# Kernel optimization log

Hardware: AMD Instinct MI355X
Metric: run time of the kernel (lower is better)

The kernel has to match this reference:

```python
import jax, jax.numpy as jnp
import numpy as np

N_NODES = 50000
N_EDGES = 500000
F_IN = 128
F_OUT = 128
N_REL = 8


def setup_inputs() -> dict:
    key = jax.random.key(0)
    ks = jax.random.split(key, 10)
    x = jax.random.normal(ks[0], (N_NODES, F_IN), dtype=jnp.float32)
    edge_index = jax.random.randint(ks[1], (2, N_EDGES), 0, N_NODES, dtype=jnp.int64)
    edge_types = jax.random.randint(ks[2], (N_EDGES,), 0, N_REL, dtype=jnp.int64)
    s = 1.0 / np.sqrt(F_IN)
    Wr = jax.random.uniform(ks[3], (N_REL, F_OUT, F_IN), jnp.float32, -s, s)  # per-relation Linear weights [out,in]
    br = jax.random.uniform(ks[4], (N_REL, F_OUT), jnp.float32, -s, s)
    Ws = jax.random.uniform(ks[5], (F_OUT, F_IN), jnp.float32, -s, s)         # self Linear
    bs = jax.random.uniform(ks[6], (F_OUT,), jnp.float32, -s, s)
    sa = 1.0 / np.sqrt(2 * F_IN)
    wa = jax.random.uniform(ks[7], (2 * F_IN,), jnp.float32, -sa, sa)         # attention Linear(2*in, 1) weight
    ba = jax.random.uniform(ks[8], (1,), jnp.float32, -sa, sa)
    return {"x": x, "edge_index": edge_index, "edge_types": edge_types,
            "Wr": Wr, "br": br, "Ws": Ws, "bs": bs, "wa": wa, "ba": ba}


def reference(x, edge_index, edge_types, Wr, br, Ws, bs, wa, ba):
    N, Fin = x.shape
    R = Wr.shape[0]
    src, tgt = edge_index[0], edge_index[1]
    # self term: self_weight(x)
    out = x @ Ws.T + bs
    # attention: sigmoid(cat(x[src], x[tgt]) @ wa + ba), decomposed per node then gathered
    a_src = x @ wa[:Fin]   # [N]
    a_tgt = x @ wa[Fin:]   # [N]
    a = jax.nn.sigmoid(a_src[src] + a_tgt[tgt] + ba[0])  # [E]
    # contribution per edge: a * (x[src] @ Wr^T + br)  =>  aggregate (a * x[src]) and a per (target, relation)
    scaled = x[src] * a[:, None]                         # [E, Fin]
    seg = tgt * R + edge_types                           # combined (target, relation) segment id
    agg = jax.ops.segment_sum(scaled, seg, num_segments=N * R).reshape(N, R, Fin)
    asum = jax.ops.segment_sum(a, seg, num_segments=N * R).reshape(N, R)
    out = out + jnp.einsum('nri,roi->no', agg, Wr) + asum @ br
    return out
```

## Files before the change

kernel.cpp:

```cpp
#include <hip/hip_runtime.h>
#include <math.h>

#define NND 50000
#define NED 500000
#define FDIM 128
#define NREL 8
#define KTOT 1152
#define MPAD 50048
#define CAP 64
#define NKC  (KTOT / 64)

typedef __attribute__((ext_vector_type(8))) short short8;
typedef __attribute__((ext_vector_type(4))) float f32x4;
typedef const void __attribute__((address_space(1)))* gptr_t;
typedef void __attribute__((address_space(3)))* lptr_t;

static __device__ __forceinline__ unsigned short f2bf(float f) {
    unsigned u = __float_as_uint(f);
    u += 0x7FFFu + ((u >> 16) & 1u);
    return (unsigned short)(u >> 16);
}
static __device__ __forceinline__ float bf2f(unsigned short b) {
    return __uint_as_float((unsigned)b << 16);
}

#define NDB   12500
#define PBB   72
#define CZB   196
#define AZB   27
__global__ void node_dots_kernel(const float* __restrict__ x,
                                 const float* __restrict__ wa,
                                 float* __restrict__ a_src,
                                 float* __restrict__ a_tgt,
                                 unsigned short* __restrict__ Abig,
                                 unsigned short* __restrict__ xb,
                                 const float* __restrict__ Ws,
                                 const float* __restrict__ Wr,
                                 unsigned short* __restrict__ Bt,
                                 int* __restrict__ counts) {
    int b = blockIdx.x;
    if (b < NDB) {
        int gid  = b * 256 + threadIdx.x;
        int node = gid >> 6;
        int lane = threadIdx.x & 63;
        float2 v = *(const float2*)(x + (size_t)node * FDIM + lane * 2);
        ushort2 vb = { f2bf(v.x), f2bf(v.y) };
        *(ushort2*)(Abig + (size_t)node * KTOT + lane * 2) = vb;
        *(ushort2*)(xb   + (size_t)node * FDIM + lane * 2) = vb;
        float s1 = v.x * wa[2 * lane]        + v.y * wa[2 * lane + 1];
        float s2 = v.x * wa[FDIM + 2 * lane] + v.y * wa[FDIM + 2 * lane + 1];
#pragma unroll
        for (int off = 32; off > 0; off >>= 1) {
            s1 += __shfl_xor(s1, off);
            s2 += __shfl_xor(s2, off);
        }
        if (lane == 0) { a_src[node] = s1; a_tgt[node] = s2; }
    } else if (b < NDB + PBB) {
        int idx0 = (b - NDB) * 2048 + threadIdx.x * 8;
        int o  = idx0 / KTOT;
        int k0 = idx0 - o * KTOT;
        unsigned short tmp[8];
#pragma unroll
        for (int j = 0; j < 8; ++j) {
            int k = k0 + j;
            float v;
            if (k < FDIM) v = Ws[o * FDIM + k];
            else {
                int r = (k - FDIM) >> 7;
                int i = (k - FDIM) & 127;
                v = Wr[((size_t)r * FDIM + o) * FDIM + i];
            }
            tmp[j] = f2bf(v);
        }
        *(short8*)(Bt + idx0) = *(short8*)tmp;
    } else if (b < NDB + PBB + CZB) {
        int i = (b - NDB - PBB) * 256 + threadIdx.x;
        if (i < NND) counts[i] = 0;
    } else {
        int i = (b - NDB - PBB - CZB) * 256 + threadIdx.x;
        float4 z = make_float4(0.f, 0.f, 0.f, 0.f);
        ((float4*)(Abig + (size_t)NND * KTOT))[i] = z;
    }
}

__global__ void scatter_kernel(const int* __restrict__ ei, const int* __restrict__ et,
                               const float* __restrict__ a_src, const float* __restrict__ a_tgt,
                               const float* __restrict__ ba,
                               int* __restrict__ counts,
                               unsigned long long* __restrict__ sorted2) {
    int e = blockIdx.x * blockDim.x + threadIdx.x;
    if (e >= NED) return;
    int src = ei[e];
    int tgt = ei[NED + e];
    int rel = et[e];
    float s = a_src[src] + a_tgt[tgt] + ba[0];
    float a = 1.0f / (1.0f + __expf(-s));
    int slot = atomicAdd(&counts[tgt], 1);
    if (slot < CAP) {
        unsigned long long pk = ((unsigned long long)__float_as_uint(a) << 32)
                              | (unsigned)((rel << 16) | src);
        sorted2[(size_t)tgt * CAP + slot] = pk;
    }
}

__global__ __launch_bounds__(256) void segsum_kernel(
        const int* __restrict__ counts, const unsigned long long* __restrict__ sorted2,
        const unsigned short* __restrict__ xb,
        unsigned short* __restrict__ Abig, float* __restrict__ asum) {
    int wid  = (blockIdx.x * blockDim.x + threadIdx.x) >> 6;
    int lane = threadIdx.x & 63;
    if (wid >= NND) return;
    int tgt = wid;
    int cnt = counts[tgt];
    if (cnt > CAP) cnt = CAP;
    const unsigned long long* seg = sorted2 + (size_t)tgt * CAP;

    float2 c0 = {0,0}, c1 = {0,0}, c2 = {0,0}, c3 = {0,0};
    float2 c4 = {0,0}, c5 = {0,0}, c6 = {0,0}, c7 = {0,0};
    float s0=0,s1=0,s2=0,s3=0,s4=0,s5=0,s6=0,s7=0;

    const ushort2* xl = (const ushort2*)xb + lane;

#define ACC(PK, W) {                                                    \
        float a  = __uint_as_float((unsigned)((PK) >> 32));             \
        int  rel = (int)(((PK) >> 16) & 0xF);                           \
        float vx = bf2f((W).x), vy = bf2f((W).y);                       \
        switch (rel) {                                                  \
            case 0: c0.x += a*vx; c0.y += a*vy; s0 += a; break;         \
            case 1: c1.x += a*vx; c1.y += a*vy; s1 += a; break;         \
            case 2: c2.x += a*vx; c2.y += a*vy; s2 += a; break;         \
            case 3: c3.x += a*vx; c3.y += a*vy; s3 += a; break;         \
            case 4: c4.x += a*vx; c4.y += a*vy; s4 += a; break;         \
            case 5: c5.x += a*vx; c5.y += a*vy; s5 += a; break;         \
            case 6: c6.x += a*vx; c6.y += a*vy; s6 += a; break;         \
            default: c7.x += a*vx; c7.y += a*vy; s7 += a; break;        \
        }                                                               \
    }

    int k = 0;
    if (cnt >= 4) {
        unsigned long long pk0 = seg[0];
        unsigned long long pk1 = seg[1];
        unsigned long long pk2 = seg[2];
        unsigned long long pk3 = seg[3];
        for (; k + 8 <= cnt; k += 4) {
            ushort2 w0 = xl[(size_t)(pk0 & 0xFFFF) * 64];
            ushort2 w1 = xl[(size_t)(pk1 & 0xFFFF) * 64];
            ushort2 w2 = xl[(size_t)(pk2 & 0xFFFF) * 64];
            ushort2 w3 = xl[(size_t)(pk3 & 0xFFFF) * 64];
            unsigned long long q0 = seg[k + 4];
            unsigned long long q1 = seg[k + 5];
            unsigned long long q2 = seg[k + 6];
            unsigned long long q3 = seg[k + 7];
            ACC(pk0, w0); ACC(pk1, w1); ACC(pk2, w2); ACC(pk3, w3);
            pk0 = q0; pk1 = q1; pk2 = q2; pk3 = q3;
        }
        ushort2 w0 = xl[(size_t)(pk0 & 0xFFFF) * 64];
        ushort2 w1 = xl[(size_t)(pk1 & 0xFFFF) * 64];
        ushort2 w2 = xl[(size_t)(pk2 & 0xFFFF) * 64];
        ushort2 w3 = xl[(size_t)(pk3 & 0xFFFF) * 64];
        ACC(pk0, w0); ACC(pk1, w1); ACC(pk2, w2); ACC(pk3, w3);
        k += 4;
    }
    for (; k < cnt; ++k) {
        unsigned long long pk = seg[k];
        ushort2 w = xl[(size_t)(pk & 0xFFFF) * 64];
        ACC(pk, w);
    }
#undef ACC

    unsigned short* base = Abig + (size_t)tgt * KTOT + FDIM + lane * 2;
    ushort2 w;
    w.x = f2bf(c0.x); w.y = f2bf(c0.y); *(ushort2*)(base + 0 * FDIM) = w;
    w.x = f2bf(c1.x); w.y = f2bf(c1.y); *(ushort2*)(base + 1 * FDIM) = w;
    w.x = f2bf(c2.x); w.y = f2bf(c2.y); *(ushort2*)(base + 2 * FDIM) = w;
    w.x = f2bf(c3.x); w.y = f2bf(c3.y); *(ushort2*)(base + 3 * FDIM) = w;
    w.x = f2bf(c4.x); w.y = f2bf(c4.y); *(ushort2*)(base + 4 * FDIM) = w;
    w.x = f2bf(c5.x); w.y = f2bf(c5.y); *(ushort2*)(base + 5 * FDIM) = w;
    w.x = f2bf(c6.x); w.y = f2bf(c6.y); *(ushort2*)(base + 6 * FDIM) = w;
    w.x = f2bf(c7.x); w.y = f2bf(c7.y); *(ushort2*)(base + 7 * FDIM) = w;
    if (lane == 0) {
        float* ab = asum + (size_t)tgt * NREL;
        ab[0]=s0; ab[1]=s1; ab[2]=s2; ab[3]=s3; ab[4]=s4; ab[5]=s5; ab[6]=s6; ab[7]=s7;
    }
}

__global__ __launch_bounds__(256) void mfma_gemm_kernel(
        const unsigned short* __restrict__ Abig,
        const unsigned short* __restrict__ Bt,
        const float* __restrict__ asum,
        const float* __restrict__ br,
        const float* __restrict__ bs,
        float* __restrict__ out) {
    __shared__ __align__(16) unsigned short AsB[64 * 64];
    __shared__ __align__(16) unsigned short BsB[128 * 64];
    int tid  = threadIdx.x;
    int wave = tid >> 6;
    int lane = tid & 63;
    int l15  = lane & 15;
    int lhi  = lane >> 4;
    int brow = blockIdx.x * 64;
    int wr = wave >> 1;
    int wc = wave & 1;

    f32x4 acc[2][4];
#pragma unroll
    for (int mi = 0; mi < 2; ++mi)
#pragma unroll
        for (int ni = 0; ni < 4; ++ni) acc[mi][ni] = (f32x4){0.f, 0.f, 0.f, 0.f};

    for (int kc = 0; kc < NKC; ++kc) {
#pragma unroll
        for (int q = 0; q < 2; ++q) {
            int c    = tid + q * 256;
            int trow = c >> 3;
            int csw  = (c & 7) ^ (trow & 7);
            const unsigned short* src = Abig + (size_t)(brow + trow) * KTOT + kc * 64 + csw * 8;
            __builtin_amdgcn_global_load_lds((gptr_t)src,
                (lptr_t)&AsB[wave * 512 + q * 2048], 16, 0, 0);
        }
#pragma unroll
        for (int q = 0; q < 4; ++q) {
            int c   = tid + q * 256;
            int o   = c >> 3;
            int csw = (c & 7) ^ (o & 7);
            const unsigned short* src = Bt + (size_t)o * KTOT + kc * 64 + csw * 8;
            __builtin_amdgcn_global_load_lds((gptr_t)src,
                (lptr_t)&BsB[wave * 512 + q * 2048], 16, 0, 0);
        }
        __syncthreads();
#pragma unroll
        for (int ks = 0; ks < 2; ++ks) {
            int kslot = ks * 4 + lhi;
            short8 a[2], b[4];
#pragma unroll
            for (int mi = 0; mi < 2; ++mi) {
                int row = wr * 32 + mi * 16 + l15;
                a[mi] = *(const short8*)&AsB[row * 64 + ((kslot ^ (row & 7)) << 3)];
            }
#pragma unroll
            for (int ni = 0; ni < 4; ++ni) {
                int o = wc * 64 + ni * 16 + l15;
                b[ni] = *(const short8*)&BsB[o * 64 + ((kslot ^ (o & 7)) << 3)];
            }
#pragma unroll
            for (int mi = 0; mi < 2; ++mi)
#pragma unroll
                for (int ni = 0; ni < 4; ++ni)
                    acc[mi][ni] = __builtin_amdgcn_mfma_f32_16x16x32_bf16(
                        a[mi], b[ni], acc[mi][ni], 0, 0, 0);
        }
        __syncthreads();
    }

#pragma unroll
    for (int mi = 0; mi < 2; ++mi) {
        int rowbase = brow + wr * 32 + mi * 16 + lhi * 4;
#pragma unroll
        for (int j = 0; j < 4; ++j) {
            int row = rowbase + j;
            if (row >= NND) continue;
            const float* as = asum + (size_t)row * NREL;
            float4 sa = *(const float4*)as;
            float4 sb = *(const float4*)(as + 4);
#pragma unroll
            for (int ni = 0; ni < 4; ++ni) {
                int col = wc * 64 + ni * 16 + l15;
                float v = acc[mi][ni][j] + bs[col];
                v += sa.x * br[0 * FDIM + col] + sa.y * br[1 * FDIM + col]
                   + sa.z * br[2 * FDIM + col] + sa.w * br[3 * FDIM + col];
                v += sb.x * br[4 * FDIM + col] + sb.y * br[5 * FDIM + col]
                   + sb.z * br[6 * FDIM + col] + sb.w * br[7 * FDIM + col];
                out[(size_t)row * FDIM + col] = v;
            }
        }
    }
}

extern "C" void kernel_launch(void* const* d_in, const int* in_sizes, int n_in,
                              void* d_out, int out_size, void* d_ws, size_t ws_size,
                              hipStream_t stream) {
    const float* x  = (const float*)d_in[0];
    const int*   ei = (const int*)d_in[1];
    const int*   et = (const int*)d_in[2];
    const float* Wr = (const float*)d_in[3];
    const float* br = (const float*)d_in[4];
    const float* Ws = (const float*)d_in[5];
    const float* bs = (const float*)d_in[6];
    const float* wa = (const float*)d_in[7];
    const float* ba = (const float*)d_in[8];
    float* out = (float*)d_out;
    float* ws  = (float*)d_ws;

    const size_t abigF = ((size_t)MPAD * KTOT) / 2;
    const size_t btF   = ((size_t)FDIM * KTOT) / 2;
    const size_t xbF   = ((size_t)NND * FDIM) / 2;
    size_t o = 0;
    unsigned short* Abig = (unsigned short*)(ws + o); o += abigF;
    unsigned short* Bt   = (unsigned short*)(ws + o); o += btF;
    unsigned short* xb   = (unsigned short*)(ws + o); o += xbF;
    float* asum  = ws + o; o += (size_t)NND * NREL;
    float* a_src = ws + o; o += NND;
    float* a_tgt = ws + o; o += NND;
    int*   counts = (int*)(ws + o); o += NND;
    unsigned long long* sorted2 = (unsigned long long*)(ws + o); o += 2 * (size_t)NND * CAP;
    if (ws_size < o * sizeof(float)) return;

    dim3 blk(256);

    node_dots_kernel<<<NDB + PBB + CZB + AZB, blk, 0, stream>>>(
        x, wa, a_src, a_tgt, Abig, xb, Ws, Wr, Bt, counts);
    scatter_kernel<<<(NED + 255) / 256, blk, 0, stream>>>(
        ei, et, a_src, a_tgt, ba, counts, sorted2);
    segsum_kernel<<<(NND + 3) / 4, blk, 0, stream>>>(counts, sorted2, xb, Abig, asum);
    mfma_gemm_kernel<<<MPAD / 64, blk, 0, stream>>>(Abig, Bt, asum, br, bs, out);
}
```

Before: 119.0 us.

## Transform nodes per relation before aggregation instead of aggregating then transforming

Reorders the computation so that a GEMM first produces per-node, per-relation transformed features Z = x·Wr^T + br (plus the self term), and the edge pass then gathers and sums Z rows weighted by attention. This removes the wide 1152-column Abig buffer, the per-relation register switch in the segment sum, and the separate asum·br epilogue. The GEMM now has K=128 with nine output slices instead of K=1152. In exchange it writes a large bf16 Z buffer (N×8×128), and the gather reads from a tensor eight times larger, which lowers cache locality. Bias is also rounded to bf16 per edge.

```diff
diff --git a/kernel.cpp b/kernel.cpp
--- a/kernel.cpp
+++ b/kernel.cpp
@@ -5,10 +5,9 @@
 #define NED 500000
 #define FDIM 128
 #define NREL 8
-#define KTOT 1152
+#define NSL 9
 #define MPAD 50048
 #define CAP 64
-#define NKC  (KTOT / 64)
 
 typedef __attribute__((ext_vector_type(8))) short short8;
 typedef __attribute__((ext_vector_type(4))) float f32x4;
@@ -25,18 +24,17 @@
 }
 
 #define NDB   12500
+#define XZB   3
 #define PBB   72
 #define CZB   196
-#define AZB   27
 __global__ void node_dots_kernel(const float* __restrict__ x,
                                  const float* __restrict__ wa,
                                  float* __restrict__ a_src,
                                  float* __restrict__ a_tgt,
-                                 unsigned short* __restrict__ Abig,
                                  unsigned short* __restrict__ xb,
                                  const float* __restrict__ Ws,
                                  const float* __restrict__ Wr,
-                                 unsigned short* __restrict__ Bt,
+                                 unsigned short* __restrict__ Bt2,
                                  int* __restrict__ counts) {
     int b = blockIdx.x;
     if (b < NDB) {
@@ -45,8 +43,7 @@
         int lane = threadIdx.x & 63;
         float2 v = *(const float2*)(x + (size_t)node * FDIM + lane * 2);
         ushort2 vb = { f2bf(v.x), f2bf(v.y) };
-        *(ushort2*)(Abig + (size_t)node * KTOT + lane * 2) = vb;
-        *(ushort2*)(xb   + (size_t)node * FDIM + lane * 2) = vb;
+        *(ushort2*)(xb + (size_t)node * FDIM + lane * 2) = vb;
         float s1 = v.x * wa[2 * lane]        + v.y * wa[2 * lane + 1];
         float s2 = v.x * wa[FDIM + 2 * lane] + v.y * wa[FDIM + 2 * lane + 1];
 #pragma unroll
@@ -55,31 +52,28 @@
             s2 += __shfl_xor(s2, off);
         }
         if (lane == 0) { a_src[node] = s1; a_tgt[node] = s2; }
-    } else if (b < NDB + PBB) {
-        int idx0 = (b - NDB) * 2048 + threadIdx.x * 8;
-        int o  = idx0 / KTOT;
-        int k0 = idx0 - o * KTOT;
+    } else if (b < NDB + XZB) {
+        int i = (b - NDB) * 256 + threadIdx.x;
+        float4 z = make_float4(0.f, 0.f, 0.f, 0.f);
+        ((float4*)(xb + (size_t)NND * FDIM))[i] = z;
+    } else if (b < NDB + XZB + PBB) {
+        int idx0 = (b - NDB - XZB) * 2048 + threadIdx.x * 8;
+        int o2 = idx0 >> 7;
+        int k0 = idx0 & 127;
+        int s  = o2 >> 7;
+        int o  = o2 & 127;
         unsigned short tmp[8];
 #pragma unroll
         for (int j = 0; j < 8; ++j) {
             int k = k0 + j;
-            float v;
-            if (k < FDIM) v = Ws[o * FDIM + k];
-            else {
-                int r = (k - FDIM) >> 7;
-                int i = (k - FDIM) & 127;
-                v = Wr[((size_t)r * FDIM + o) * FDIM + i];
-            }
+            float v = (s == 0) ? Ws[o * FDIM + k]
+                               : Wr[(((size_t)(s - 1) * FDIM) + o) * FDIM + k];
             tmp[j] = f2bf(v);
         }
-        *(short8*)(Bt + idx0) = *(short8*)tmp;
-    } else if (b < NDB + PBB + CZB) {
-        int i = (b - NDB - PBB) * 256 + threadIdx.x;
+        *(short8*)(Bt2 + idx0) = *(short8*)tmp;
+    } else {
+        int i = (b - NDB - XZB - PBB) * 256 + threadIdx.x;
         if (i < NND) counts[i] = 0;
-    } else {
-        int i = (b - NDB - PBB - CZB) * 256 + threadIdx.x;
-        float4 z = make_float4(0.f, 0.f, 0.f, 0.f);
-        ((float4*)(Abig + (size_t)NND * KTOT))[i] = z;
     }
 }
 
@@ -103,94 +97,12 @@
     }
 }
 
-__global__ __launch_bounds__(256) void segsum_kernel(
-        const int* __restrict__ counts, const unsigned long long* __restrict__ sorted2,
+__global__ __launch_bounds__(256) void gemm_z_kernel(
         const unsigned short* __restrict__ xb,
-        unsigned short* __restrict__ Abig, float* __restrict__ asum) {
-    int wid  = (blockIdx.x * blockDim.x + threadIdx.x) >> 6;
-    int lane = threadIdx.x & 63;
-    if (wid >= NND) return;
-    int tgt = wid;
-    int cnt = counts[tgt];
-    if (cnt > CAP) cnt = CAP;
-    const unsigned long long* seg = sorted2 + (size_t)tgt * CAP;
-
-    float2 c0 = {0,0}, c1 = {0,0}, c2 = {0,0}, c3 = {0,0};
-    float2 c4 = {0,0}, c5 = {0,0}, c6 = {0,0}, c7 = {0,0};
-    float s0=0,s1=0,s2=0,s3=0,s4=0,s5=0,s6=0,s7=0;
-
-    const ushort2* xl = (const ushort2*)xb + lane;
-
-#define ACC(PK, W) {                                                    \
-        float a  = __uint_as_float((unsigned)((PK) >> 32));             \
-        int  rel = (int)(((PK) >> 16) & 0xF);                           \
-        float vx = bf2f((W).x), vy = bf2f((W).y);                       \
-        switch (rel) {                                                  \
-            case 0: c0.x += a*vx; c0.y += a*vy; s0 += a; break;         \
-            case 1: c1.x += a*vx; c1.y += a*vy; s1 += a; break;         \
-            case 2: c2.x += a*vx; c2.y += a*vy; s2 += a; break;         \
-            case 3: c3.x += a*vx; c3.y += a*vy; s3 += a; break;         \
-            case 4: c4.x += a*vx; c4.y += a*vy; s4 += a; break;         \
-            case 5: c5.x += a*vx; c5.y += a*vy; s5 += a; break;         \
-            case 6: c6.x += a*vx; c6.y += a*vy; s6 += a; break;         \
-            default: c7.x += a*vx; c7.y += a*vy; s7 += a; break;        \
-        }                                                               \
-    }
-
-    int k = 0;
-    if (cnt >= 4) {
-        unsigned long long pk0 = seg[0];
-        unsigned long long pk1 = seg[1];
-        unsigned long long pk2 = seg[2];
-        unsigned long long pk3 = seg[3];
-        for (; k + 8 <= cnt; k += 4) {
-            ushort2 w0 = xl[(size_t)(pk0 & 0xFFFF) * 64];
-            ushort2 w1 = xl[(size_t)(pk1 & 0xFFFF) * 64];
-            ushort2 w2 = xl[(size_t)(pk2 & 0xFFFF) * 64];
-            ushort2 w3 = xl[(size_t)(pk3 & 0xFFFF) * 64];
-            unsigned long long q0 = seg[k + 4];
-            unsigned long long q1 = seg[k + 5];
-            unsigned long long q2 = seg[k + 6];
-            unsigned long long q3 = seg[k + 7];
-            ACC(pk0, w0); ACC(pk1, w1); ACC(pk2, w2); ACC(pk3, w3);
-            pk0 = q0; pk1 = q1; pk2 = q2; pk3 = q3;
-        }
-        ushort2 w0 = xl[(size_t)(pk0 & 0xFFFF) * 64];
-        ushort2 w1 = xl[(size_t)(pk1 & 0xFFFF) * 64];
-        ushort2 w2 = xl[(size_t)(pk2 & 0xFFFF) * 64];
-        ushort2 w3 = xl[(size_t)(pk3 & 0xFFFF) * 64];
-        ACC(pk0, w0); ACC(pk1, w1); ACC(pk2, w2); ACC(pk3, w3);
-        k += 4;
-    }
-    for (; k < cnt; ++k) {
-        unsigned long long pk = seg[k];
-        ushort2 w = xl[(size_t)(pk & 0xFFFF) * 64];
-        ACC(pk, w);
-    }
-#undef ACC
-
-    unsigned short* base = Abig + (size_t)tgt * KTOT + FDIM + lane * 2;
-    ushort2 w;
-    w.x = f2bf(c0.x); w.y = f2bf(c0.y); *(ushort2*)(base + 0 * FDIM) = w;
-    w.x = f2bf(c1.x); w.y = f2bf(c1.y); *(ushort2*)(base + 1 * FDIM) = w;
-    w.x = f2bf(c2.x); w.y = f2bf(c2.y); *(ushort2*)(base + 2 * FDIM) = w;
-    w.x = f2bf(c3.x); w.y = f2bf(c3.y); *(ushort2*)(base + 3 * FDIM) = w;
-    w.x = f2bf(c4.x); w.y = f2bf(c4.y); *(ushort2*)(base + 4 * FDIM) = w;
-    w.x = f2bf(c5.x); w.y = f2bf(c5.y); *(ushort2*)(base + 5 * FDIM) = w;
-    w.x = f2bf(c6.x); w.y = f2bf(c6.y); *(ushort2*)(base + 6 * FDIM) = w;
-    w.x = f2bf(c7.x); w.y = f2bf(c7.y); *(ushort2*)(base + 7 * FDIM) = w;
-    if (lane == 0) {
-        float* ab = asum + (size_t)tgt * NREL;
-        ab[0]=s0; ab[1]=s1; ab[2]=s2; ab[3]=s3; ab[4]=s4; ab[5]=s5; ab[6]=s6; ab[7]=s7;
-    }
-}
-
-__global__ __launch_bounds__(256) void mfma_gemm_kernel(
-        const unsigned short* __restrict__ Abig,
-        const unsigned short* __restrict__ Bt,
-        const float* __restrict__ asum,
+        const unsigned short* __restrict__ Bt2,
         const float* __restrict__ br,
         const float* __restrict__ bs,
+        unsigned short* __restrict__ Z,
         float* __restrict__ out) {
     __shared__ __align__(16) unsigned short AsB[64 * 64];
     __shared__ __align__(16) unsigned short BsB[128 * 64];
@@ -199,7 +111,10 @@
     int lane = tid & 63;
     int l15  = lane & 15;
     int lhi  = lane >> 4;
-    int brow = blockIdx.x * 64;
+    int bid  = blockIdx.x;
+    int mtile = bid / NSL;
+    int slice = bid - mtile * NSL;
+    int brow = mtile * 64;
     int wr = wave >> 1;
     int wc = wave & 1;
 
@@ -209,13 +124,13 @@
 #pragma unroll
         for (int ni = 0; ni < 4; ++ni) acc[mi][ni] = (f32x4){0.f, 0.f, 0.f, 0.f};
 
-    for (int kc = 0; kc < NKC; ++kc) {
+    for (int kc = 0; kc < 2; ++kc) {
 #pragma unroll
         for (int q = 0; q < 2; ++q) {
             int c    = tid + q * 256;
             int trow = c >> 3;
             int csw  = (c & 7) ^ (trow & 7);
-            const unsigned short* src = Abig + (size_t)(brow + trow) * KTOT + kc * 64 + csw * 8;
+            const unsigned short* src = xb + (size_t)(brow + trow) * FDIM + kc * 64 + csw * 8;
             __builtin_amdgcn_global_load_lds((gptr_t)src,
                 (lptr_t)&AsB[wave * 512 + q * 2048], 16, 0, 0);
         }
@@ -224,7 +139,7 @@
             int c   = tid + q * 256;
             int o   = c >> 3;
             int csw = (c & 7) ^ (o & 7);
-            const unsigned short* src = Bt + (size_t)o * KTOT + kc * 64 + csw * 8;
+            const unsigned short* src = Bt2 + ((size_t)slice * FDIM + o) * FDIM + kc * 64 + csw * 8;
             __builtin_amdgcn_global_load_lds((gptr_t)src,
                 (lptr_t)&BsB[wave * 512 + q * 2048], 16, 0, 0);
         }
@@ -253,28 +168,100 @@
         __syncthreads();
     }
 
-#pragma unroll
-    for (int mi = 0; mi < 2; ++mi) {
-        int rowbase = brow + wr * 32 + mi * 16 + lhi * 4;
-#pragma unroll
-        for (int j = 0; j < 4; ++j) {
-            int row = rowbase + j;
-            if (row >= NND) continue;
-            const float* as = asum + (size_t)row * NREL;
-            float4 sa = *(const float4*)as;
-            float4 sb = *(const float4*)(as + 4);
-#pragma unroll
-            for (int ni = 0; ni < 4; ++ni) {
-                int col = wc * 64 + ni * 16 + l15;
-                float v = acc[mi][ni][j] + bs[col];
-                v += sa.x * br[0 * FDIM + col] + sa.y * br[1 * FDIM + col]
-                   + sa.z * br[2 * FDIM + col] + sa.w * br[3 * FDIM + col];
-                v += sb.x * br[4 * FDIM + col] + sb.y * br[5 * FDIM + col]
-                   + sb.z * br[6 * FDIM + col] + sb.w * br[7 * FDIM + col];
-                out[(size_t)row * FDIM + col] = v;
+    if (slice == 0) {
+#pragma unroll
+        for (int mi = 0; mi < 2; ++mi) {
+            int rowbase = brow + wr * 32 + mi * 16 + lhi * 4;
+#pragma unroll
+            for (int j = 0; j < 4; ++j) {
+                int row = rowbase + j;
+                if (row >= NND) continue;
+#pragma unroll
+                for (int ni = 0; ni < 4; ++ni) {
+                    int col = wc * 64 + ni * 16 + l15;
+                    out[(size_t)row * FDIM + col] = acc[mi][ni][j] + bs[col];
+                }
             }
         }
-    }
+    } else {
+        const float* brr = br + (size_t)(slice - 1) * FDIM;
+        unsigned short* zb = Z + (size_t)(slice - 1) * FDIM;
+#pragma unroll
+        for (int mi = 0; mi < 2; ++mi) {
+            int rowbase = brow + wr * 32 + mi * 16 + lhi * 4;
+#pragma unroll
+            for (int j = 0; j < 4; ++j) {
+                int row = rowbase + j;
+#pragma unroll
+                for (int ni = 0; ni < 4; ++ni) {
+                    int col = wc * 64 + ni * 16 + l15;
+                    zb[(size_t)row * (NREL * FDIM) + col] = f2bf(acc[mi][ni][j] + brr[col]);
+                }
+            }
+        }
+    }
+}
+
+__global__ __launch_bounds__(256) void edge_agg_kernel(
+        const int* __restrict__ counts, const unsigned long long* __restrict__ sorted2,
+        const unsigned short* __restrict__ Z,
+        float* __restrict__ out) {
+    int wid  = (blockIdx.x * blockDim.x + threadIdx.x) >> 6;
+    int lane = threadIdx.x & 63;
+    if (wid >= NND) return;
+    int tgt = wid;
+    int cnt = counts[tgt];
+    if (cnt > CAP) cnt = CAP;
+    const unsigned long long* seg = sorted2 + (size_t)tgt * CAP;
+
+    float2 c = {0.f, 0.f};
+    const ushort2* zl = (const ushort2*)Z + lane;
+
+#define ACC(PK, W) {                                                    \
+        float a  = __uint_as_float((unsigned)((PK) >> 32));             \
+        c.x += a * bf2f((W).x);                                         \
+        c.y += a * bf2f((W).y);                                         \
+    }
+#define ZIDX(PK) ((size_t)((((PK) & 0xFFFFu) << 3) | (((PK) >> 16) & 7u)) * 64)
+
+    int k = 0;
+    if (cnt >= 4) {
+        unsigned long long pk0 = seg[0];
+        unsigned long long pk1 = seg[1];
+        unsigned long long pk2 = seg[2];
+        unsigned long long pk3 = seg[3];
+        for (; k + 8 <= cnt; k += 4) {
+            ushort2 w0 = zl[ZIDX(pk0)];
+            ushort2 w1 = zl[ZIDX(pk1)];
+            ushort2 w2 = zl[ZIDX(pk2)];
+            ushort2 w3 = zl[ZIDX(pk3)];
+            unsigned long long q0 = seg[k + 4];
+            unsigned long long q1 = seg[k + 5];
+            unsigned long long q2 = seg[k + 6];
+            unsigned long long q3 = seg[k + 7];
+            ACC(pk0, w0); ACC(pk1, w1); ACC(pk2, w2); ACC(pk3, w3);
+            pk0 = q0; pk1 = q1; pk2 = q2; pk3 = q3;
+        }
+        ushort2 w0 = zl[ZIDX(pk0)];
+        ushort2 w1 = zl[ZIDX(pk1)];
+        ushort2 w2 = zl[ZIDX(pk2)];
+        ushort2 w3 = zl[ZIDX(pk3)];
+        ACC(pk0, w0); ACC(pk1, w1); ACC(pk2, w2); ACC(pk3, w3);
+        k += 4;
+    }
+    for (; k < cnt; ++k) {
+        unsigned long long pk = seg[k];
+        ushort2 w = zl[ZIDX(pk)];
+        ACC(pk, w);
+    }
+#undef ACC
+#undef ZIDX
+
+    float2* op = (float2*)(out + (size_t)tgt * FDIM) + lane;
+    float2 v = *op;
+    v.x += c.x;
+    v.y += c.y;
+    *op = v;
 }
 
 extern "C" void kernel_launch(void* const* d_in, const int* in_sizes, int n_in,
@@ -292,14 +279,13 @@
     float* out = (float*)d_out;
     float* ws  = (float*)d_ws;
 
-    const size_t abigF = ((size_t)MPAD * KTOT) / 2;
-    const size_t btF   = ((size_t)FDIM * KTOT) / 2;
-    const size_t xbF   = ((size_t)NND * FDIM) / 2;
+    const size_t xbF  = ((size_t)MPAD * FDIM) / 2;
+    const size_t btF  = ((size_t)NSL * FDIM * FDIM) / 2;
+    const size_t zF   = ((size_t)MPAD * NREL * FDIM) / 2;
     size_t o = 0;
-    unsigned short* Abig = (unsigned short*)(ws + o); o += abigF;
-    unsigned short* Bt   = (unsigned short*)(ws + o); o += btF;
-    unsigned short* xb   = (unsigned short*)(ws + o); o += xbF;
-    float* asum  = ws + o; o += (size_t)NND * NREL;
+    unsigned short* xb  = (unsigned short*)(ws + o); o += xbF;
+    unsigned short* Bt2 = (unsigned short*)(ws + o); o += btF;
+    unsigned short* Z   = (unsigned short*)(ws + o); o += zF;
     float* a_src = ws + o; o += NND;
     float* a_tgt = ws + o; o += NND;
     int*   counts = (int*)(ws + o); o += NND;
@@ -308,10 +294,10 @@
 
     dim3 blk(256);
 
-    node_dots_kernel<<<NDB + PBB + CZB + AZB, blk, 0, stream>>>(
-        x, wa, a_src, a_tgt, Abig, xb, Ws, Wr, Bt, counts);
+    node_dots_kernel<<<NDB + XZB + PBB + CZB, blk, 0, stream>>>(
+        x, wa, a_src, a_tgt, xb, Ws, Wr, Bt2, counts);
     scatter_kernel<<<(NED + 255) / 256, blk, 0, stream>>>(
         ei, et, a_src, a_tgt, ba, counts, sorted2);
-    segsum_kernel<<<(NND + 3) / 4, blk, 0, stream>>>(counts, sorted2, xb, Abig, asum);
-    mfma_gemm_kernel<<<MPAD / 64, blk, 0, stream>>>(Abig, Bt, asum, br, bs, out);
-}
+    gemm_z_kernel<<<(MPAD / 64) * NSL, blk, 0, stream>>>(xb, Bt2, br, bs, Z, out);
+    edge_agg_kernel<<<(NND + 3) / 4, blk, 0, stream>>>(counts, sorted2, Z, out);
+}
```

Result: faster. 113.5 us (-4.6%).
